# Performance work log

Measured on AMD Instinct MI355X. Metric: run time of the kernel, lower is better.

## Reference

```python
import jax, jax.numpy as jnp
import numpy as np

D2 = 200  # 2*100 hardcoded in BiAttentionLayer.__init__
NEG = -10000000.0


def masked_softmax(v, m):
    # Faithful to the torch masked_softmax: softmax(v * m), re-mask, renormalize.
    r = jax.nn.softmax(v * m, axis=-1)
    r = r * m
    return r / (jnp.sum(r, axis=-1, keepdims=True) + 1e-13)


def setup_inputs() -> dict:
    key = jax.random.key(0)
    k0, k1, k2, k3, k4, k5 = jax.random.split(key, 6)
    N, T, J = 64, 1024, 64
    H = jax.random.normal(k0, (N, T, D2), jnp.float32)
    U = jax.random.normal(k1, (N, J, D2), jnp.float32)
    c_mask = jax.random.randint(k2, (N, T), 0, 2).astype(jnp.float32)
    q_mask = jax.random.randint(k3, (N, J), 0, 2).astype(jnp.float32)
    w = jax.random.normal(k4, (3 * D2,), jnp.float32) * 0.05  # Linear(3*d2, 1) weight
    b = jax.random.normal(k5, (), jnp.float32) * 0.05          # Linear bias
    return {"H": H, "U": U, "c_mask": c_mask, "q_mask": q_mask, "w": w, "b": b}


def reference(H, U, c_mask, q_mask, w, b):
    # Similarity: linear over concat(h, u, h*u) decomposed so the (N,T,J,3d)
    # intermediate is never materialized (same math as the torch module).
    w_h, w_u, w_hu = w[:D2], w[D2:2 * D2], w[2 * D2:]
    S = ((H @ w_h)[:, :, None]
         + (U @ w_u)[:, None, :]
         + jnp.einsum('ntd,njd->ntj', H * w_hu, U)
         + b)  # [N,T,J]

    # C2Q: masked softmax over question dim, attend over U.
    S_t = masked_softmax(S, q_mask[:, None, :])        # [N,T,J]
    U_ = jnp.einsum('ntj,njd->ntd', S_t, U)            # [N,T,d2]

    # Q2C: replace masked values with -1e7, max over J, softmax over context dim.
    qm = q_mask[:, None, :]
    S_rep = S * qm + NEG * (1.0 - qm)                  # [N,T,J]
    S_max = jnp.max(S_rep, axis=-1)                    # [N,T]
    a = masked_softmax(S_max, c_mask)                  # [N,T]
    H_ = jnp.einsum('nt,ntd->nd', a, H)[:, None, :]    # [N,1,d2] (broadcasts over T)

    G = jnp.concatenate([H, U_, H * U_, H * H_], axis=-1)  # [N,T,4*d2]
    return G
```

## Files before the change

kernel.cpp:

```cpp
#include <hip/hip_runtime.h>
#include <stdint.h>

#define NEGV -10000000.0f

typedef __attribute__((ext_vector_type(8))) short short8;
typedef __attribute__((ext_vector_type(4))) float f32x4;

__device__ __forceinline__ ushort f2b(float f) {
    uint32_t x = __float_as_uint(f);
    uint32_t r = x + 0x7FFFu + ((x >> 16) & 1u);
    return (ushort)(r >> 16);
}
__device__ __forceinline__ float b2f(ushort u) {
    union { float f; uint32_t i; } v; v.i = ((uint32_t)u) << 16; return v.f;
}

__launch_bounds__(256)
__global__ void k0_prep(const float* __restrict__ Ug, const float* __restrict__ wg,
                        const float* __restrict__ bg,
                        ushort* __restrict__ Bf, ushort* __restrict__ Uf,
                        float* __restrict__ cW) {
    __shared__ __align__(16) float sU[64][204];
    __shared__ float sW[600];
    const int tid = threadIdx.x, lane = tid & 63, wid = tid >> 6;
    const int n = blockIdx.x;

    for (int i = tid; i < 600; i += 256) sW[i] = wg[i];
    for (int r = wid; r < 64; r += 4) {
        const float* urow = Ug + (size_t)(n * 64 + r) * 200;
        if (lane < 50) *(float4*)&sU[r][lane * 4] = *(const float4*)(urow + lane * 4);
    }
    __syncthreads();
    const float bval = bg[0];

    ushort* bfn = Bf + (size_t)n * (28 * 512);
    for (int item = tid; item < 28 * 64; item += 256) {
        int chunk = item >> 6, l2 = item & 63;
        int kc = chunk >> 2, jt = chunk & 3;
        int g2 = l2 >> 4, li2 = l2 & 15;
        int j = jt * 16 + li2;
        int d0 = kc * 32 + g2 * 8;
        short8 v;
        #pragma unroll
        for (int e = 0; e < 8; ++e) {
            int d = d0 + e;
            float bh = 0.f;
            if (d < 200) bh = sU[j][d] * sW[400 + d] + sW[d];
            v[e] = (short)f2b(bh);
        }
        *(short8*)(bfn + (size_t)item * 8) = v;
    }

    ushort* ufn = Uf + (size_t)n * (26 * 512);
    for (int item = tid; item < 26 * 64; item += 256) {
        int chunk = item >> 6, l2 = item & 63;
        int kc2 = chunk / 13, dt = chunk % 13;
        int g2 = l2 >> 4, li2 = l2 & 15;
        int d = dt * 16 + li2;
        int j0 = kc2 * 32 + g2 * 8;
        short8 v;
        #pragma unroll
        for (int e = 0; e < 8; ++e)
            v[e] = (d < 200) ? (short)f2b(sU[j0 + e][d]) : (short)0;
        *(short8*)(ufn + (size_t)item * 8) = v;
    }

    for (int r = wid; r < 64; r += 4) {
        float part = 0.f;
        for (int d = lane; d < 200; d += 64) part += sU[r][d] * sW[200 + d];
        #pragma unroll
        for (int off = 32; off >= 1; off >>= 1) part += __shfl_xor(part, off);
        if (lane == 0) cW[n * 64 + r] = part + bval;
    }
}

__launch_bounds__(64, 4)
__global__ void kA_gemm1(const float* __restrict__ Hg,
                         const ushort* __restrict__ Bf,
                         const float* __restrict__ cW,
                         const float* __restrict__ qmg,
                         ushort* __restrict__ PfW,
                         float* __restrict__ SmaxWs) {
    __shared__ __align__(16) ushort sHb[16][232];
    __shared__ __align__(16) ushort sP[16][80];
    const int lane = threadIdx.x;
    const int g = lane >> 4, li = lane & 15;
    const int n = blockIdx.y, t0 = blockIdx.x * 16;

    const float* Hbase = Hg + (size_t)(n * 1024 + t0) * 200;
    #pragma unroll
    for (int it = 0; it < 13; ++it) {
        int idx = lane + it * 64;
        if (idx < 800) {
            int row = idx / 50, c4 = (idx - row * 50) * 4;
            float4 h = *(const float4*)(Hbase + (size_t)row * 200 + c4);
            uint2 wv;
            wv.x = ((uint)f2b(h.y) << 16) | (uint)f2b(h.x);
            wv.y = ((uint)f2b(h.w) << 16) | (uint)f2b(h.z);
            *(uint2*)&sHb[row][c4] = wv;
        }
    }
    #pragma unroll
    for (int it = 0; it < 4; ++it) {
        int id2 = lane + it * 64;
        int row = id2 >> 4, c = id2 & 15;
        *(uint*)&sHb[row][200 + c * 2] = 0u;
    }

    const ushort* Bn = Bf + (size_t)n * (28 * 512);
    f32x4 acc[4];
    #pragma unroll
    for (int jt = 0; jt < 4; ++jt) acc[jt] = (f32x4){0.f, 0.f, 0.f, 0.f};
    const ushort* aRow = &sHb[li][g * 8];

    short8 bbuf[2][4];
    #pragma unroll
    for (int jt = 0; jt < 4; ++jt)
        bbuf[0][jt] = *(const short8*)(Bn + (size_t)((0 * 4 + jt) * 64 + lane) * 8);
    #pragma unroll
    for (int kc = 0; kc < 7; ++kc) {
        if (kc < 6) {
            #pragma unroll
            for (int jt = 0; jt < 4; ++jt)
                bbuf[(kc + 1) & 1][jt] =
                    *(const short8*)(Bn + (size_t)(((kc + 1) * 4 + jt) * 64 + lane) * 8);
        }
        short8 av = *(const short8*)(aRow + kc * 32);
        #pragma unroll
        for (int jt = 0; jt < 4; ++jt)
            acc[jt] = __builtin_amdgcn_mfma_f32_16x16x32_bf16(av, bbuf[kc & 1][jt],
                                                              acc[jt], 0, 0, 0);
    }

    float cj[4], qm[4];
    #pragma unroll
    for (int jt = 0; jt < 4; ++jt) {
        cj[jt] = cW[n * 64 + jt * 16 + li];
        qm[jt] = qmg[n * 64 + jt * 16 + li];
    }
    #pragma unroll
    for (int reg = 0; reg < 4; ++reg) {
        float x[4], y[4];
        float xm = -1e30f, ym = -1e30f;
        #pragma unroll
        for (int jt = 0; jt < 4; ++jt) {
            float s = acc[jt][reg] + cj[jt];
            x[jt] = s * qm[jt];
            y[jt] = (qm[jt] != 0.f) ? s : NEGV;
            xm = fmaxf(xm, x[jt]); ym = fmaxf(ym, y[jt]);
        }
        #pragma unroll
        for (int off = 1; off <= 8; off <<= 1) {
            xm = fmaxf(xm, __shfl_xor(xm, off));
            ym = fmaxf(ym, __shfl_xor(ym, off));
        }
        float e[4], z = 0.f, zm = 0.f;
        #pragma unroll
        for (int jt = 0; jt < 4; ++jt) {
            e[jt] = __expf(x[jt] - xm);
            z += e[jt]; zm += e[jt] * qm[jt];
        }
        #pragma unroll
        for (int off = 1; off <= 8; off <<= 1) {
            z  += __shfl_xor(z, off);
            zm += __shfl_xor(zm, off);
        }
        float inv = 1.f / (zm + 1e-13f * z);
        int trow = g * 4 + reg;
        #pragma unroll
        for (int jt = 0; jt < 4; ++jt) sP[trow][jt * 16 + li] = f2b(e[jt] * qm[jt] * inv);
        if (li == 0) SmaxWs[n * 1024 + t0 + trow] = ym;
    }

    ushort* pf = PfW + (size_t)(n * 64 + blockIdx.x) * 1024;
    #pragma unroll
    for (int c2 = 0; c2 < 2; ++c2) {
        short8 v = *(const short8*)&sP[lane & 15][c2 * 32 + (lane >> 4) * 8];
        *(short8*)(pf + c2 * 512 + lane * 8) = v;
    }
}

__launch_bounds__(256)
__global__ void k2a_softmaxT(const float* __restrict__ cmg,
                             const float* __restrict__ SmaxWs,
                             float* __restrict__ aWs,
                             float* __restrict__ HbarWs) {
    __shared__ float red[8];
    const int tid = threadIdx.x, lane = tid & 63, wid = tid >> 6;
    const int n = blockIdx.x;

    float x[4], m[4];
    #pragma unroll
    for (int i = 0; i < 4; ++i) {
        int t = tid + 256 * i;
        float v = SmaxWs[n * 1024 + t];
        m[i] = cmg[(size_t)n * 1024 + t];
        x[i] = v * m[i];
    }
    float mx = fmaxf(fmaxf(x[0], x[1]), fmaxf(x[2], x[3]));
    #pragma unroll
    for (int off = 32; off >= 1; off >>= 1) mx = fmaxf(mx, __shfl_xor(mx, off));
    if (lane == 0) red[wid] = mx;
    __syncthreads();
    float M = fmaxf(fmaxf(red[0], red[1]), fmaxf(red[2], red[3]));
    __syncthreads();
    float e[4], z = 0.f, zm = 0.f;
    #pragma unroll
    for (int i = 0; i < 4; ++i) {
        e[i] = __expf(x[i] - M);
        z += e[i]; zm += e[i] * m[i];
    }
    #pragma unroll
    for (int off = 32; off >= 1; off >>= 1) {
        z  += __shfl_xor(z, off);
        zm += __shfl_xor(zm, off);
    }
    if (lane == 0) { red[wid] = z; red[4 + wid] = zm; }
    __syncthreads();
    float Z  = red[0] + red[1] + red[2] + red[3];
    float Zm = red[4] + red[5] + red[6] + red[7];
    float inv = 1.f / (Zm + 1e-13f * Z);
    #pragma unroll
    for (int i = 0; i < 4; ++i) aWs[n * 1024 + tid + 256 * i] = e[i] * m[i] * inv;
    if (tid < 200) HbarWs[n * 200 + tid] = 0.f;
}

__launch_bounds__(256)
__global__ void k2b_hbar(const float* __restrict__ Hg,
                         const float* __restrict__ aWs,
                         float* __restrict__ HbarWs) {
    __shared__ float sA[64];
    const int tid = threadIdx.x;
    const int n = blockIdx.y, t0 = blockIdx.x * 64;
    if (tid < 64) sA[tid] = aWs[n * 1024 + t0 + tid];
    __syncthreads();
    if (tid < 200) {
        const float* hp = Hg + (size_t)(n * 1024 + t0) * 200 + tid;
        float acc = 0.f;
        #pragma unroll 8
        for (int t = 0; t < 64; ++t) acc += sA[t] * hp[(size_t)t * 200];
        atomicAdd(HbarWs + n * 200 + tid, acc);
    }
}

__launch_bounds__(256, 4)
__global__ void kB_gemm2_out(const float* __restrict__ Hg,
                             const ushort* __restrict__ Uf,
                             const ushort* __restrict__ PfW,
                             const float* __restrict__ HbarWs,
                             float* __restrict__ Gout) {
    __shared__ __align__(16) ushort sU2[64][208];
    const int tid = threadIdx.x, lane = tid & 63, w = tid >> 6;
    const int g = lane >> 4, li = lane & 15;
    const int n = blockIdx.y, r0 = blockIdx.x * 64;
    const int tIdx = blockIdx.x * 4 + w;

    const ushort* pf = PfW + (size_t)(n * 64 + tIdx) * 1024;
    const ushort* Un = Uf + (size_t)n * (26 * 512);
    f32x4 acc2[13];
    #pragma unroll
    for (int dt = 0; dt < 13; ++dt) acc2[dt] = (f32x4){0.f, 0.f, 0.f, 0.f};
    #pragma unroll
    for (int kc2 = 0; kc2 < 2; ++kc2) {
        short8 a2 = *(const short8*)(pf + kc2 * 512 + lane * 8);
        #pragma unroll
        for (int dt = 0; dt < 13; ++dt) {
            short8 bv = *(const short8*)(Un + (size_t)((kc2 * 13 + dt) * 64 + lane) * 8);
            acc2[dt] = __builtin_amdgcn_mfma_f32_16x16x32_bf16(a2, bv, acc2[dt], 0, 0, 0);
        }
    }

    #pragma unroll
    for (int dt = 0; dt < 13; ++dt) {
        int d = dt * 16 + li;
        if (d < 200) {
            #pragma unroll
            for (int reg = 0; reg < 4; ++reg)
                sU2[w * 16 + g * 4 + reg][d] = f2b(acc2[dt][reg]);
        }
    }

    const int d0 = lane * 4;
    f32x4 hbv = (f32x4){0.f, 0.f, 0.f, 0.f};
    if (lane < 50) hbv = *(const f32x4*)(HbarWs + n * 200 + d0);

    for (int rr = 0; rr < 16; ++rr) {
        int r = w * 16 + rr;
        if (lane < 50) {
            const float* hrow = Hg + (size_t)(n * 1024 + r0 + r) * 200;
            float* orow = Gout + (size_t)(n * 1024 + r0 + r) * 800;
            f32x4 h = *(const f32x4*)(hrow + d0);
            uint2 uraw = *(const uint2*)&sU2[r][d0];
            f32x4 u;
            u[0] = b2f((ushort)(uraw.x & 0xffffu)); u[1] = b2f((ushort)(uraw.x >> 16));
            u[2] = b2f((ushort)(uraw.y & 0xffffu)); u[3] = b2f((ushort)(uraw.y >> 16));
            f32x4 hu = h * u;
            f32x4 hh = h * hbv;
            __builtin_nontemporal_store(h,  (f32x4*)(orow + d0));
            __builtin_nontemporal_store(u,  (f32x4*)(orow + 200 + d0));
            __builtin_nontemporal_store(hu, (f32x4*)(orow + 400 + d0));
            __builtin_nontemporal_store(hh, (f32x4*)(orow + 600 + d0));
        }
    }
}

extern "C" void kernel_launch(void* const* d_in, const int* in_sizes, int n_in,
                              void* d_out, int out_size, void* d_ws, size_t ws_size,
                              hipStream_t stream) {
    (void)in_sizes; (void)n_in; (void)out_size; (void)ws_size;
    const float* Hg  = (const float*)d_in[0];
    const float* Ug  = (const float*)d_in[1];
    const float* cmg = (const float*)d_in[2];
    const float* qmg = (const float*)d_in[3];
    const float* wg  = (const float*)d_in[4];
    const float* bg  = (const float*)d_in[5];
    float* Gout = (float*)d_out;

    char* ws = (char*)d_ws;
    float*  SmaxWs = (float*) (ws);
    float*  aWs    = (float*) (ws + 262144);
    float*  HbarWs = (float*) (ws + 524288);
    float*  cWs    = (float*) (ws + 575488);
    ushort* BfWs   = (ushort*)(ws + 591872);
    ushort* UfWs   = (ushort*)(ws + 2426880);
    ushort* PfWs   = (ushort*)(ws + 4130816);

    dim3 blk256(256, 1, 1);
    k0_prep<<<dim3(64, 1, 1), blk256, 0, stream>>>(Ug, wg, bg, BfWs, UfWs, cWs);
    kA_gemm1<<<dim3(64, 64, 1), dim3(64, 1, 1), 0, stream>>>(Hg, BfWs, cWs, qmg,
                                                             PfWs, SmaxWs);
    k2a_softmaxT<<<dim3(64, 1, 1), blk256, 0, stream>>>(cmg, SmaxWs, aWs, HbarWs);
    k2b_hbar<<<dim3(16, 64, 1), blk256, 0, stream>>>(Hg, aWs, HbarWs);
    kB_gemm2_out<<<dim3(16, 64, 1), blk256, 0, stream>>>(Hg, UfWs, PfWs, HbarWs, Gout);
}
```

Measured before the change: 309.3 us.

## Fuse Q2C context softmax and Hbar into gemm1 via online-softmax partials

The Q2C softmax over context and the weighted sum of H are folded into kA_gemm1. Each 16-row tile computes a local max, partial sums and a bf16 partial weighted H vector from its shared-memory H copy. A small combine kernel rescales and merges the 64 partials per batch, replacing two kernels, a second full read of H, and the atomics. In exchange, Hbar is now built from bf16-rounded H and a bf16 partial sum, which lowers precision.

Result: no change. 306.1 us (-1.1%).

```diff
diff --git a/kernel.cpp b/kernel.cpp
--- a/kernel.cpp
+++ b/kernel.cpp
@@ -79,10 +79,16 @@
                          const ushort* __restrict__ Bf,
                          const float* __restrict__ cW,
                          const float* __restrict__ qmg,
+                         const float* __restrict__ cmg,
                          ushort* __restrict__ PfW,
-                         float* __restrict__ SmaxWs) {
+                         ushort* __restrict__ vPart,
+                         float* __restrict__ partM,
+                         float* __restrict__ partZ,
+                         float* __restrict__ partZm) {
     __shared__ __align__(16) ushort sHb[16][232];
     __shared__ __align__(16) ushort sP[16][80];
+    __shared__ float sYm[16];
+    __shared__ float sCm[16];
     const int lane = threadIdx.x;
     const int g = lane >> 4, li = lane & 15;
     const int n = blockIdx.y, t0 = blockIdx.x * 16;
@@ -106,6 +112,7 @@
         int row = id2 >> 4, c = id2 & 15;
         *(uint*)&sHb[row][200 + c * 2] = 0u;
     }
+    if (lane < 16) sCm[lane] = cmg[(size_t)n * 1024 + t0 + lane];
 
     const ushort* Bn = Bf + (size_t)n * (28 * 512);
     f32x4 acc[4];
@@ -169,7 +176,7 @@
         int trow = g * 4 + reg;
         #pragma unroll
         for (int jt = 0; jt < 4; ++jt) sP[trow][jt * 16 + li] = f2b(e[jt] * qm[jt] * inv);
-        if (li == 0) SmaxWs[n * 1024 + t0 + trow] = ym;
+        if (li == 0) sYm[trow] = ym;
     }
 
     ushort* pf = PfW + (size_t)(n * 64 + blockIdx.x) * 1024;
@@ -178,68 +185,69 @@
         short8 v = *(const short8*)&sP[lane & 15][c2 * 32 + (lane >> 4) * 8];
         *(short8*)(pf + c2 * 512 + lane * 8) = v;
     }
+
+    float m_c = -1e30f;
+    #pragma unroll
+    for (int t = 0; t < 16; ++t) m_c = fmaxf(m_c, sYm[t] * sCm[t]);
+    float z = 0.f, zm = 0.f;
+    f32x4 v = (f32x4){0.f, 0.f, 0.f, 0.f};
+    const int d0 = (lane < 50) ? lane * 4 : 0;
+    #pragma unroll
+    for (int t = 0; t < 16; ++t) {
+        float e = __expf(sYm[t] * sCm[t] - m_c);
+        z += e;
+        float wt = e * sCm[t];
+        zm += wt;
+        uint2 raw = *(const uint2*)&sHb[t][d0];
+        v[0] += wt * b2f((ushort)(raw.x & 0xffffu));
+        v[1] += wt * b2f((ushort)(raw.x >> 16));
+        v[2] += wt * b2f((ushort)(raw.y & 0xffffu));
+        v[3] += wt * b2f((ushort)(raw.y >> 16));
+    }
+    const int tile = n * 64 + blockIdx.x;
+    if (lane < 50) {
+        uint2 pv;
+        pv.x = ((uint)f2b(v[1]) << 16) | (uint)f2b(v[0]);
+        pv.y = ((uint)f2b(v[3]) << 16) | (uint)f2b(v[2]);
+        *(uint2*)(vPart + (size_t)tile * 200 + lane * 4) = pv;
+    }
+    if (lane == 0) { partM[tile] = m_c; partZ[tile] = z; partZm[tile] = zm; }
 }
 
 __launch_bounds__(256)
-__global__ void k2a_softmaxT(const float* __restrict__ cmg,
-                             const float* __restrict__ SmaxWs,
-                             float* __restrict__ aWs,
-                             float* __restrict__ HbarWs) {
-    __shared__ float red[8];
-    const int tid = threadIdx.x, lane = tid & 63, wid = tid >> 6;
+__global__ void kC_combine(const ushort* __restrict__ vPart,
+                           const float* __restrict__ partM,
+                           const float* __restrict__ partZ,
+                           const float* __restrict__ partZm,
+                           float* __restrict__ HbarWs) {
+    __shared__ float sF[64];
+    __shared__ float sInv;
+    const int tid = threadIdx.x;
     const int n = blockIdx.x;
 
-    float x[4], m[4];
-    #pragma unroll
-    for (int i = 0; i < 4; ++i) {
-        int t = tid + 256 * i;
-        float v = SmaxWs[n * 1024 + t];
-        m[i] = cmg[(size_t)n * 1024 + t];
-        x[i] = v * m[i];
-    }
-    float mx = fmaxf(fmaxf(x[0], x[1]), fmaxf(x[2], x[3]));
-    #pragma unroll
-    for (int off = 32; off >= 1; off >>= 1) mx = fmaxf(mx, __shfl_xor(mx, off));
-    if (lane == 0) red[wid] = mx;
-    __syncthreads();
-    float M = fmaxf(fmaxf(red[0], red[1]), fmaxf(red[2], red[3]));
-    __syncthreads();
-    float e[4], z = 0.f, zm = 0.f;
-    #pragma unroll
-    for (int i = 0; i < 4; ++i) {
-        e[i] = __expf(x[i] - M);
-        z += e[i]; zm += e[i] * m[i];
-    }
-    #pragma unroll
-    for (int off = 32; off >= 1; off >>= 1) {
-        z  += __shfl_xor(z, off);
-        zm += __shfl_xor(zm, off);
-    }
-    if (lane == 0) { red[wid] = z; red[4 + wid] = zm; }
-    __syncthreads();
-    float Z  = red[0] + red[1] + red[2] + red[3];
-    float Zm = red[4] + red[5] + red[6] + red[7];
-    float inv = 1.f / (Zm + 1e-13f * Z);
-    #pragma unroll
-    for (int i = 0; i < 4; ++i) aWs[n * 1024 + tid + 256 * i] = e[i] * m[i] * inv;
-    if (tid < 200) HbarWs[n * 200 + tid] = 0.f;
-}
-
-__launch_bounds__(256)
-__global__ void k2b_hbar(const float* __restrict__ Hg,
-                         const float* __restrict__ aWs,
-                         float* __restrict__ HbarWs) {
-    __shared__ float sA[64];
-    const int tid = threadIdx.x;
-    const int n = blockIdx.y, t0 = blockIdx.x * 64;
-    if (tid < 64) sA[tid] = aWs[n * 1024 + t0 + tid];
+    if (tid < 64) {
+        float mc  = partM[n * 64 + tid];
+        float zc  = partZ[n * 64 + tid];
+        float zmc = partZm[n * 64 + tid];
+        float M = mc;
+        #pragma unroll
+        for (int off = 32; off >= 1; off >>= 1) M = fmaxf(M, __shfl_xor(M, off));
+        float f = __expf(mc - M);
+        sF[tid] = f;
+        float Zc = zc * f, Zmc = zmc * f;
+        #pragma unroll
+        for (int off = 32; off >= 1; off >>= 1) {
+            Zc  += __shfl_xor(Zc, off);
+            Zmc += __shfl_xor(Zmc, off);
+        }
+        if (tid == 0) sInv = 1.f / (Zmc + 1e-13f * Zc);
+    }
     __syncthreads();
     if (tid < 200) {
-        const float* hp = Hg + (size_t)(n * 1024 + t0) * 200 + tid;
         float acc = 0.f;
-        #pragma unroll 8
-        for (int t = 0; t < 64; ++t) acc += sA[t] * hp[(size_t)t * 200];
-        atomicAdd(HbarWs + n * 200 + tid, acc);
+        for (int c = 0; c < 64; ++c)
+            acc += b2f(vPart[(size_t)(n * 64 + c) * 200 + tid]) * sF[c];
+        HbarWs[n * 200 + tid] = acc * sInv;
     }
 }
 
@@ -317,19 +325,22 @@
     float* Gout = (float*)d_out;
 
     char* ws = (char*)d_ws;
-    float*  SmaxWs = (float*) (ws);
-    float*  aWs    = (float*) (ws + 262144);
-    float*  HbarWs = (float*) (ws + 524288);
-    float*  cWs    = (float*) (ws + 575488);
-    ushort* BfWs   = (ushort*)(ws + 591872);
-    ushort* UfWs   = (ushort*)(ws + 2426880);
-    ushort* PfWs   = (ushort*)(ws + 4130816);
+    float*  HbarWs = (float*) (ws);
+    float*  cWs    = (float*) (ws + 51200);
+    float*  partM  = (float*) (ws + 67584);
+    float*  partZ  = (float*) (ws + 83968);
+    float*  partZm = (float*) (ws + 100352);
+    ushort* vPart  = (ushort*)(ws + 116736);
+    ushort* BfWs   = (ushort*)(ws + 1755136);
+    ushort* UfWs   = (ushort*)(ws + 3590144);
+    ushort* PfWs   = (ushort*)(ws + 5294080);
 
     dim3 blk256(256, 1, 1);
     k0_prep<<<dim3(64, 1, 1), blk256, 0, stream>>>(Ug, wg, bg, BfWs, UfWs, cWs);
-    kA_gemm1<<<dim3(64, 64, 1), dim3(64, 1, 1), 0, stream>>>(Hg, BfWs, cWs, qmg,
-                                                             PfWs, SmaxWs);
-    k2a_softmaxT<<<dim3(64, 1, 1), blk256, 0, stream>>>(cmg, SmaxWs, aWs, HbarWs);
-    k2b_hbar<<<dim3(16, 64, 1), blk256, 0, stream>>>(Hg, aWs, HbarWs);
+    kA_gemm1<<<dim3(64, 64, 1), dim3(64, 1, 1), 0, stream>>>(Hg, BfWs, cWs, qmg, cmg,
+                                                             PfWs, vPart, partM,
+                                                             partZ, partZm);
+    kC_combine<<<dim3(64, 1, 1), blk256, 0, stream>>>(vPart, partM, partZ, partZm,
+                                                      HbarWs);
     kB_gemm2_out<<<dim3(16, 64, 1), blk256, 0, stream>>>(Hg, UfWs, PfWs, HbarWs, Gout);
 }
```
